# Optimization experiments

Hardware: AMD Instinct MI355X
Metric: run time of the kernel (lower is better)

The kernel has to match this reference:

```python
import jax, jax.numpy as jnp
import numpy as np

NUM_RING = 16
MAX_RING = 1520
EPS = 1e-5


def setup_inputs() -> dict:
    key = jax.random.key(0)
    B, C, N = 16, 64, 16384
    cnt = N // NUM_RING  # 1024 points per ring, sorted
    k1, k2, k3, k4, k5 = jax.random.split(key, 5)
    x = jax.random.normal(k1, (B, C, N), dtype=jnp.float32)
    # ring ids: sorted, exactly cnt points per ring (the module assumes sorted,
    # identical-count rings across batch)
    ring = jnp.broadcast_to(jnp.arange(N, dtype=jnp.int64) // cnt, (B, N))
    # random-upsample indices: concat(arange(cnt), randperm(cnt)[:MAX_RING-cnt])
    rng = np.random.default_rng(0)
    up = MAX_RING - cnt  # 496
    choice = np.empty((B, NUM_RING, MAX_RING), dtype=np.int64)
    for b in range(B):
        for r in range(NUM_RING):
            choice[b, r, :cnt] = np.arange(cnt)
            choice[b, r, cnt:] = rng.permutation(cnt)[:up]
    choice = jnp.asarray(choice)
    # grouped Conv1d(64 -> 128, kernel 1, groups=16): weight [128, 4, 1] -> [16, 8, 4]
    Wg = jax.random.normal(k2, (NUM_RING, 8, 4), dtype=jnp.float32) * 0.5
    bias = jax.random.normal(k3, (128,), dtype=jnp.float32) * 0.1
    gamma = jnp.ones((128,), dtype=jnp.float32)
    beta = jnp.zeros((128,), dtype=jnp.float32)
    return {"x": x, "Wg": Wg, "bias": bias, "gamma": gamma, "beta": beta,
            "ring": ring, "choice": choice}


def reference(x, Wg, bias, gamma, beta, ring, choice):
    B, C, N = x.shape  # C = 64
    R, MR = NUM_RING, MAX_RING
    cnt = N // R
    L = R * MR  # 24320

    xt = jnp.transpose(x, (0, 2, 1))  # [B, N, 64]
    # per-ring gather with random upsample to MAX_RING points
    idx = (jnp.arange(R, dtype=choice.dtype)[None, :, None] * cnt + choice)  # [B,R,MR]
    gathered = jnp.take_along_axis(xt, idx.reshape(B, L, 1), axis=1)  # [B, L, 64]

    # faithful to torch: cat(...).view(B, 64, -1) is a raw reshape (channel-scrambling)
    xc = gathered.reshape(B, C, L)  # [B, 64, L]

    # grouped 1x1 conv: 16 groups, 4 in / 8 out channels each
    xg = xc.reshape(B, R, 4, L)
    y = jnp.einsum('goc,bgcl->bgol', Wg, xg).reshape(B, 128, L)
    y = y + bias[None, :, None]

    # BatchNorm1d (training mode: batch statistics, biased variance)
    mean = jnp.mean(y, axis=(0, 2))
    var = jnp.var(y, axis=(0, 2))
    y = gamma[None, :, None] * (y - mean[None, :, None]) * jax.lax.rsqrt(var + EPS)[None, :, None] + beta[None, :, None]

    # per-ring max over MAX_RING slots, broadcast back to original ring sizes
    pooled = jnp.max(y.reshape(B, 128, R, MR), axis=-1)  # [B, 128, R]
    out = jnp.repeat(pooled, cnt, axis=2)  # [B, 128, N]
    return out
```

## Files before the change

kernel.cpp:

```cpp
#include <hip/hip_runtime.h>
#include <float.h>

#define NB    16
#define CIN   64
#define NPT   16384
#define NRING 16
#define MAXR  1520
#define LTOT  (NRING*MAXR)
#define MBLK  380
#define NCH   128
#define NBLK1 (NB*CIN*4)
#define MW    380

__device__ __forceinline__ float sload(float v) {
    return __int_as_float(__builtin_amdgcn_readfirstlane(__float_as_int(v)));
}

__global__ __launch_bounds__(256) void k1_gather_conv(
    const float* __restrict__ x, const float* __restrict__ Wg,
    const float* __restrict__ bias, const float* __restrict__ gamma,
    const int* __restrict__ choice,
    float* __restrict__ p_sum, float* __restrict__ p_sqs,
    float* __restrict__ p_max)
{
    __shared__ float xs[4096];
    __shared__ int   iw[4*MW];

    const int blk = blockIdx.x;
    const int b  = blk >> 8;
    const int cp = (blk >> 2) & 63;
    const int q  = blk & 3;
    const int t  = threadIdx.x;

    {
        const float4* src = (const float4*)(x + ((size_t)(b*CIN + cp)) * NPT + q*4096);
        float4* dst = (float4*)xs;
        #pragma unroll
        for (int i = 0; i < 4; ++i) dst[t + i*256] = src[t + i*256];
    }
    {
        const int g4 = t >> 6, lane = t & 63;
        const int* __restrict__ cg = choice + ((size_t)(b*NRING + q*4 + g4)) * MAXR;
        #pragma unroll
        for (int k = 0; k < 6; ++k) {
            const int m = lane + k*64;
            if (m < MW) {
                const int c2 = cg[760  + m];
                const int c3 = cg[1140 + m];
                iw[g4*MW + m] = c2 | (c3 << 16);
            }
        }
    }
    __syncthreads();

    const int g4   = t >> 6;
    const int lane = t & 63;
    const int r    = lane >> 2;
    const int s    = lane & 3;
    const int g    = q*4 + g4;

    float w[8][4], bs[8];
    #pragma unroll
    for (int o = 0; o < 8; ++o) {
        const int ch = g*8 + o;
        const float sg = (gamma[ch] < 0.0f) ? -1.0f : 1.0f;
        bs[o] = sload(sg * bias[ch]);
        #pragma unroll
        for (int c = 0; c < 4; ++c) w[o][c] = sload(sg * Wg[ch*4 + c]);
    }

    const int mlo = (r*MAXR - cp + 63) >> 6;
    int mhi = ((r+1)*MAXR - cp + 63) >> 6;
    if (mhi > MBLK) mhi = MBLK;

    const float* __restrict__ xg = xs + (g4 << 10);
    const int*   __restrict__ ig = iw + g4*MW;

    float smax[8], ssum[8], ssq[8];
    #pragma unroll
    for (int o = 0; o < 8; ++o) { smax[o] = -FLT_MAX; ssum[o] = 0.f; ssq[o] = 0.f; }

    const int m0 = mlo + s;

    int wv[5];
    #pragma unroll
    for (int k = 0; k < 5; ++k) wv[k] = ig[m0 + 4*k];

    #pragma unroll
    for (int k = 0; k < 5; ++k) {
        const int m = m0 + 4*k;
        const int i2 = wv[k] & 0xFFFF;
        const int i3 = ((unsigned)wv[k]) >> 16;
        const float v0 = xg[m];
        const float v1 = xg[380 + m];
        const float v2 = xg[i2];
        const float v3 = xg[i3];
        #pragma unroll
        for (int o = 0; o < 8; ++o) {
            float y = fmaf(w[o][0], v0, fmaf(w[o][1], v1,
                      fmaf(w[o][2], v2, fmaf(w[o][3], v3, bs[o]))));
            smax[o] = fmaxf(smax[o], y);
            ssum[o] += y;
            ssq[o]  = fmaf(y, y, ssq[o]);
        }
    }
    {
        const int m = m0 + 20;
        if (m < mhi) {
            const int wt = ig[m];
            const int i2 = wt & 0xFFFF;
            const int i3 = ((unsigned)wt) >> 16;
            const float v0 = xg[m];
            const float v1 = xg[380 + m];
            const float v2 = xg[i2];
            const float v3 = xg[i3];
            #pragma unroll
            for (int o = 0; o < 8; ++o) {
                float y = fmaf(w[o][0], v0, fmaf(w[o][1], v1,
                          fmaf(w[o][2], v2, fmaf(w[o][3], v3, bs[o]))));
                smax[o] = fmaxf(smax[o], y);
                ssum[o] += y;
                ssq[o]  = fmaf(y, y, ssq[o]);
            }
        }
    }

    #pragma unroll
    for (int o = 0; o < 8; ++o) {
        smax[o] = fmaxf(smax[o], __shfl_xor(smax[o], 1));
        ssum[o] += __shfl_xor(ssum[o], 1);
        ssq[o]  += __shfl_xor(ssq[o], 1);
        smax[o] = fmaxf(smax[o], __shfl_xor(smax[o], 2));
        ssum[o] += __shfl_xor(ssum[o], 2);
        ssq[o]  += __shfl_xor(ssq[o], 2);
    }

    if (s == 0) {
        float* base = p_max + (((size_t)(b*64 + cp))*NRING + r)*NCH + q*32 + g4*8;
        ((float4*)base)[0] = make_float4(smax[0], smax[1], smax[2], smax[3]);
        ((float4*)base)[1] = make_float4(smax[4], smax[5], smax[6], smax[7]);
    }

    __syncthreads();
    float* redS = xs;
    float* redQ = xs + 600;
    if (s == 0) {
        #pragma unroll
        for (int o = 0; o < 8; ++o) {
            redS[(g4*8+o)*17 + r] = ssum[o];
            redQ[(g4*8+o)*17 + r] = ssq[o];
        }
    }
    __syncthreads();
    if (t < 32) {
        float S = 0.f, Q = 0.f;
        #pragma unroll
        for (int rr = 0; rr < 16; ++rr) {
            S += redS[t*17 + rr];
            Q += redQ[t*17 + rr];
        }
        const float sg = (gamma[q*32 + t] < 0.0f) ? -1.0f : 1.0f;
        p_sum[(size_t)blk*32 + t] = sg * S;
        p_sqs[(size_t)blk*32 + t] = Q;
    }
}

__global__ __launch_bounds__(256) void k23_pool_bcast(
    const float* __restrict__ p_sum, const float* __restrict__ p_sqs,
    const float* __restrict__ p_max,
    const float* __restrict__ gamma, const float* __restrict__ beta,
    float4* __restrict__ out)
{
    __shared__ float part[16][17];
    __shared__ float wsum[4], wsq[4];
    __shared__ float pool[16];
    const int bc = blockIdx.x;
    const int b  = bc >> 7;
    const int ch = bc & 127;
    const int t  = threadIdx.x;
    const int q  = ch >> 5, c32 = ch & 31;

    const int r = t >> 4, ck = t & 15;
    float v = -FLT_MAX;
    #pragma unroll
    for (int k = 0; k < 4; ++k) {
        const int cpi = ck*4 + k;
        v = fmaxf(v, p_max[(((size_t)(b*64 + cpi))*NRING + r)*NCH + ch]);
    }

    float S = 0.f, Q = 0.f;
    #pragma unroll
    for (int i = 0; i < 4; ++i) {
        const int jj = t + i*256;
        const int b2 = jj >> 6, cp2 = jj & 63;
        const int kb = ((b2*64 + cp2) << 2) | q;
        S += p_sum[(size_t)kb*32 + c32];
        Q += p_sqs[(size_t)kb*32 + c32];
    }
    #pragma unroll
    for (int off = 1; off < 64; off <<= 1) {
        S += __shfl_xor(S, off);
        Q += __shfl_xor(Q, off);
    }
    part[r][ck] = v;
    if ((t & 63) == 0) { wsum[t >> 6] = S; wsq[t >> 6] = Q; }
    __syncthreads();

    if (t < 16) {
        const float inv = 1.0f / (float)((size_t)NB * LTOT);
        const float Sa = wsum[0] + wsum[1] + wsum[2] + wsum[3];
        const float Qa = wsq[0] + wsq[1] + wsq[2] + wsq[3];
        const float mean = Sa * inv;
        const float var  = Qa * inv - mean*mean;
        const float istd = rsqrtf(var + 1e-5f);
        float acc = part[t][0];
        #pragma unroll
        for (int k = 1; k < 16; ++k) acc = fmaxf(acc, part[t][k]);
        const float gm = gamma[ch];
        const float raw = (gm >= 0.0f) ? acc : -acc;
        pool[t] = gm * (raw - mean) * istd + beta[ch];
    }
    __syncthreads();

    float4* __restrict__ dst = out + (size_t)bc * (NPT/4);
    #pragma unroll
    for (int i = 0; i < 16; ++i) {
        const int idx = t + i*256;
        const float vv = pool[idx >> 8];
        dst[idx] = make_float4(vv, vv, vv, vv);
    }
}

extern "C" void kernel_launch(void* const* d_in, const int* in_sizes, int n_in,
                              void* d_out, int out_size, void* d_ws, size_t ws_size,
                              hipStream_t stream)
{
    const float* x     = (const float*)d_in[0];
    const float* Wg    = (const float*)d_in[1];
    const float* bias  = (const float*)d_in[2];
    const float* gamma = (const float*)d_in[3];
    const float* beta  = (const float*)d_in[4];
    const int* choice  = (const int*)d_in[6];

    float* p_sum = (float*)d_ws;
    float* p_sqs = p_sum + (size_t)NBLK1*32;
    float* p_max = p_sqs + (size_t)NBLK1*32;

    k1_gather_conv<<<NBLK1, 256, 0, stream>>>(x, Wg, bias, gamma, choice,
                                              p_sum, p_sqs, p_max);
    k23_pool_bcast<<<NB*NCH, 256, 0, stream>>>(p_sum, p_sqs, p_max,
                                               gamma, beta, (float4*)d_out);
}
```

Measured before the change: 66.39 us.

## Double-buffer x tiles via direct global-to-LDS loads and loop over channel slices

Restructures the gather-conv kernel from 4096 small 256-thread blocks into 512 blocks of 512 threads. Each block handles 8 ring groups and iterates over 4 input channel slices, reusing the loaded weights and choice indices across iterations. It double-buffers the x slices in LDS using the global_load_lds builtin, so the next slice loads while the current one is computed. Partial-sum reduction is moved to wave shuffles instead of a shared-memory pass, and the output broadcast uses nontemporal stores. The trade-offs are fewer blocks, which may leave CUs underfilled, and more LDS per block.

```diff
diff --git a/kernel.cpp b/kernel.cpp
--- a/kernel.cpp
+++ b/kernel.cpp
@@ -9,167 +9,192 @@
 #define LTOT  (NRING*MAXR)
 #define MBLK  380
 #define NCH   128
-#define NBLK1 (NB*CIN*4)
 #define MW    380
+
+typedef float fx4 __attribute__((ext_vector_type(4)));
 
 __device__ __forceinline__ float sload(float v) {
     return __int_as_float(__builtin_amdgcn_readfirstlane(__float_as_int(v)));
 }
 
-__global__ __launch_bounds__(256) void k1_gather_conv(
+#if __has_builtin(__builtin_amdgcn_global_load_lds)
+#define HAVE_GLDS 1
+__device__ __forceinline__ void gl_lds16(const float* g, float* l) {
+    __builtin_amdgcn_global_load_lds(
+        (const __attribute__((address_space(1))) void*)g,
+        (__attribute__((address_space(3))) void*)l, 16, 0, 0);
+}
+#else
+#define HAVE_GLDS 0
+#endif
+
+__global__ __launch_bounds__(512) void k1_gather_conv(
     const float* __restrict__ x, const float* __restrict__ Wg,
     const float* __restrict__ bias, const float* __restrict__ gamma,
     const int* __restrict__ choice,
     float* __restrict__ p_sum, float* __restrict__ p_sqs,
     float* __restrict__ p_max)
 {
-    __shared__ float xs[4096];
-    __shared__ int   iw[4*MW];
-
-    const int blk = blockIdx.x;
-    const int b  = blk >> 8;
-    const int cp = (blk >> 2) & 63;
-    const int q  = blk & 3;
-    const int t  = threadIdx.x;
+    __shared__ float xs[2][8192];
+    __shared__ int   iw[8*MW];
+
+    const int bid  = blockIdx.x;
+    const int bh    = bid >> 4;
+    const int slice = bid & 15;
+    const int b  = bh >> 1;
+    const int h  = bh & 1;
+    const int cp0 = slice << 2;
+    const int t    = threadIdx.x;
+    const int w    = t >> 6;
+    const int lane = t & 63;
+
+#if HAVE_GLDS
+    #define STAGE(bufi, cpv) do { \
+        const float* gb_ = x + ((size_t)(b*CIN + (cpv)))*NPT + h*8192 + w*1024 + lane*4; \
+        float* lb_ = &xs[bufi][w*1024]; \
+        gl_lds16(gb_,       lb_);       \
+        gl_lds16(gb_ + 256, lb_ + 256); \
+        gl_lds16(gb_ + 512, lb_ + 512); \
+        gl_lds16(gb_ + 768, lb_ + 768); \
+    } while (0)
+#else
+    #define STAGE(bufi, cpv) do { \
+        const fx4* src_ = (const fx4*)(x + ((size_t)(b*CIN + (cpv)))*NPT + h*8192); \
+        fx4* dst_ = (fx4*)xs[bufi]; \
+        _Pragma("unroll") \
+        for (int i_ = 0; i_ < 4; ++i_) dst_[t + i_*512] = src_[t + i_*512]; \
+    } while (0)
+#endif
+
+    STAGE(0, cp0);
 
     {
-        const float4* src = (const float4*)(x + ((size_t)(b*CIN + cp)) * NPT + q*4096);
-        float4* dst = (float4*)xs;
-        #pragma unroll
-        for (int i = 0; i < 4; ++i) dst[t + i*256] = src[t + i*256];
-    }
-    {
-        const int g4 = t >> 6, lane = t & 63;
-        const int* __restrict__ cg = choice + ((size_t)(b*NRING + q*4 + g4)) * MAXR;
+        const int* __restrict__ cg = choice + ((size_t)(b*NRING + h*8 + w))*MAXR;
         #pragma unroll
         for (int k = 0; k < 6; ++k) {
             const int m = lane + k*64;
-            if (m < MW) {
-                const int c2 = cg[760  + m];
-                const int c3 = cg[1140 + m];
-                iw[g4*MW + m] = c2 | (c3 << 16);
-            }
-        }
-    }
-    __syncthreads();
-
-    const int g4   = t >> 6;
-    const int lane = t & 63;
-    const int r    = lane >> 2;
-    const int s    = lane & 3;
-    const int g    = q*4 + g4;
-
-    float w[8][4], bs[8];
+            if (m < MW) iw[w*MW + m] = cg[760 + m] | (cg[1140 + m] << 16);
+        }
+    }
+
+    const int g = h*8 + w;
+    float wq[8][4], bq[8], sg8[8];
     #pragma unroll
     for (int o = 0; o < 8; ++o) {
         const int ch = g*8 + o;
-        const float sg = (gamma[ch] < 0.0f) ? -1.0f : 1.0f;
-        bs[o] = sload(sg * bias[ch]);
-        #pragma unroll
-        for (int c = 0; c < 4; ++c) w[o][c] = sload(sg * Wg[ch*4 + c]);
-    }
-
-    const int mlo = (r*MAXR - cp + 63) >> 6;
-    int mhi = ((r+1)*MAXR - cp + 63) >> 6;
-    if (mhi > MBLK) mhi = MBLK;
-
-    const float* __restrict__ xg = xs + (g4 << 10);
-    const int*   __restrict__ ig = iw + g4*MW;
-
-    float smax[8], ssum[8], ssq[8];
-    #pragma unroll
-    for (int o = 0; o < 8; ++o) { smax[o] = -FLT_MAX; ssum[o] = 0.f; ssq[o] = 0.f; }
-
-    const int m0 = mlo + s;
-
-    int wv[5];
-    #pragma unroll
-    for (int k = 0; k < 5; ++k) wv[k] = ig[m0 + 4*k];
-
-    #pragma unroll
-    for (int k = 0; k < 5; ++k) {
-        const int m = m0 + 4*k;
-        const int i2 = wv[k] & 0xFFFF;
-        const int i3 = ((unsigned)wv[k]) >> 16;
-        const float v0 = xg[m];
-        const float v1 = xg[380 + m];
-        const float v2 = xg[i2];
-        const float v3 = xg[i3];
-        #pragma unroll
-        for (int o = 0; o < 8; ++o) {
-            float y = fmaf(w[o][0], v0, fmaf(w[o][1], v1,
-                      fmaf(w[o][2], v2, fmaf(w[o][3], v3, bs[o]))));
-            smax[o] = fmaxf(smax[o], y);
-            ssum[o] += y;
-            ssq[o]  = fmaf(y, y, ssq[o]);
-        }
-    }
-    {
-        const int m = m0 + 20;
-        if (m < mhi) {
-            const int wt = ig[m];
-            const int i2 = wt & 0xFFFF;
-            const int i3 = ((unsigned)wt) >> 16;
+        const float sgn = (gamma[ch] < 0.0f) ? -1.0f : 1.0f;
+        sg8[o] = sload(sgn);
+        bq[o]  = sload(sgn * bias[ch]);
+        #pragma unroll
+        for (int c = 0; c < 4; ++c) wq[o][c] = sload(sgn * Wg[ch*4 + c]);
+    }
+
+    const int r = lane >> 2;
+    const int s = lane & 3;
+    const int* __restrict__ igw = iw + w*MW;
+
+    __syncthreads();
+
+    for (int tt = 0; tt < 4; ++tt) {
+        const int cp = cp0 + tt;
+        const float* __restrict__ xg = &xs[tt & 1][w << 10];
+        if (tt < 3) STAGE((tt + 1) & 1, cp + 1);
+
+        const int mlo = (r*MAXR - cp + 63) >> 6;
+        int mhi = ((r+1)*MAXR - cp + 63) >> 6;
+        if (mhi > MBLK) mhi = MBLK;
+        const int m0 = mlo + s;
+
+        int wv[5];
+        #pragma unroll
+        for (int k = 0; k < 5; ++k) wv[k] = igw[m0 + 4*k];
+
+        float smax[8], ssum[8], ssq[8];
+        #pragma unroll
+        for (int o = 0; o < 8; ++o) { smax[o] = -FLT_MAX; ssum[o] = 0.f; ssq[o] = 0.f; }
+
+        #pragma unroll
+        for (int k = 0; k < 5; ++k) {
+            const int m = m0 + 4*k;
+            const int i2 = wv[k] & 0xFFFF;
+            const int i3 = ((unsigned)wv[k]) >> 16;
             const float v0 = xg[m];
             const float v1 = xg[380 + m];
             const float v2 = xg[i2];
             const float v3 = xg[i3];
             #pragma unroll
             for (int o = 0; o < 8; ++o) {
-                float y = fmaf(w[o][0], v0, fmaf(w[o][1], v1,
-                          fmaf(w[o][2], v2, fmaf(w[o][3], v3, bs[o]))));
+                float y = fmaf(wq[o][0], v0, fmaf(wq[o][1], v1,
+                          fmaf(wq[o][2], v2, fmaf(wq[o][3], v3, bq[o]))));
                 smax[o] = fmaxf(smax[o], y);
                 ssum[o] += y;
                 ssq[o]  = fmaf(y, y, ssq[o]);
             }
         }
-    }
-
-    #pragma unroll
-    for (int o = 0; o < 8; ++o) {
-        smax[o] = fmaxf(smax[o], __shfl_xor(smax[o], 1));
-        ssum[o] += __shfl_xor(ssum[o], 1);
-        ssq[o]  += __shfl_xor(ssq[o], 1);
-        smax[o] = fmaxf(smax[o], __shfl_xor(smax[o], 2));
-        ssum[o] += __shfl_xor(ssum[o], 2);
-        ssq[o]  += __shfl_xor(ssq[o], 2);
-    }
-
-    if (s == 0) {
-        float* base = p_max + (((size_t)(b*64 + cp))*NRING + r)*NCH + q*32 + g4*8;
-        ((float4*)base)[0] = make_float4(smax[0], smax[1], smax[2], smax[3]);
-        ((float4*)base)[1] = make_float4(smax[4], smax[5], smax[6], smax[7]);
-    }
-
-    __syncthreads();
-    float* redS = xs;
-    float* redQ = xs + 600;
-    if (s == 0) {
+        {
+            const int m = m0 + 20;
+            if (m < mhi) {
+                const int wt = igw[m];
+                const int i2 = wt & 0xFFFF;
+                const int i3 = ((unsigned)wt) >> 16;
+                const float v0 = xg[m];
+                const float v1 = xg[380 + m];
+                const float v2 = xg[i2];
+                const float v3 = xg[i3];
+                #pragma unroll
+                for (int o = 0; o < 8; ++o) {
+                    float y = fmaf(wq[o][0], v0, fmaf(wq[o][1], v1,
+                              fmaf(wq[o][2], v2, fmaf(wq[o][3], v3, bq[o]))));
+                    smax[o] = fmaxf(smax[o], y);
+                    ssum[o] += y;
+                    ssq[o]  = fmaf(y, y, ssq[o]);
+                }
+            }
+        }
+
         #pragma unroll
         for (int o = 0; o < 8; ++o) {
-            redS[(g4*8+o)*17 + r] = ssum[o];
-            redQ[(g4*8+o)*17 + r] = ssq[o];
-        }
-    }
-    __syncthreads();
-    if (t < 32) {
-        float S = 0.f, Q = 0.f;
-        #pragma unroll
-        for (int rr = 0; rr < 16; ++rr) {
-            S += redS[t*17 + rr];
-            Q += redQ[t*17 + rr];
-        }
-        const float sg = (gamma[q*32 + t] < 0.0f) ? -1.0f : 1.0f;
-        p_sum[(size_t)blk*32 + t] = sg * S;
-        p_sqs[(size_t)blk*32 + t] = Q;
-    }
+            smax[o] = fmaxf(smax[o], __shfl_xor(smax[o], 1));
+            ssum[o] += __shfl_xor(ssum[o], 1);
+            ssq[o]  += __shfl_xor(ssq[o], 1);
+            smax[o] = fmaxf(smax[o], __shfl_xor(smax[o], 2));
+            ssum[o] += __shfl_xor(ssum[o], 2);
+            ssq[o]  += __shfl_xor(ssq[o], 2);
+        }
+
+        if (s == 0) {
+            float* base = p_max + (((size_t)(b*64 + cp))*NRING + r)*NCH + h*64 + w*8;
+            ((float4*)base)[0] = make_float4(smax[0], smax[1], smax[2], smax[3]);
+            ((float4*)base)[1] = make_float4(smax[4], smax[5], smax[6], smax[7]);
+        }
+
+        #pragma unroll
+        for (int o = 0; o < 8; ++o) {
+            #pragma unroll
+            for (int off = 4; off < 64; off <<= 1) {
+                ssum[o] += __shfl_xor(ssum[o], off);
+                ssq[o]  += __shfl_xor(ssq[o], off);
+            }
+        }
+        if (lane == 0) {
+            float* baseS = p_sum + ((size_t)((b*64 + cp)*2 + h))*64 + w*8;
+            float* baseQ = p_sqs + ((size_t)((b*64 + cp)*2 + h))*64 + w*8;
+            ((float4*)baseS)[0] = make_float4(sg8[0]*ssum[0], sg8[1]*ssum[1], sg8[2]*ssum[2], sg8[3]*ssum[3]);
+            ((float4*)baseS)[1] = make_float4(sg8[4]*ssum[4], sg8[5]*ssum[5], sg8[6]*ssum[6], sg8[7]*ssum[7]);
+            ((float4*)baseQ)[0] = make_float4(ssq[0], ssq[1], ssq[2], ssq[3]);
+            ((float4*)baseQ)[1] = make_float4(ssq[4], ssq[5], ssq[6], ssq[7]);
+        }
+
+        __syncthreads();
+    }
+    #undef STAGE
 }
 
 __global__ __launch_bounds__(256) void k23_pool_bcast(
     const float* __restrict__ p_sum, const float* __restrict__ p_sqs,
     const float* __restrict__ p_max,
     const float* __restrict__ gamma, const float* __restrict__ beta,
-    float4* __restrict__ out)
+    fx4* __restrict__ out)
 {
     __shared__ float part[16][17];
     __shared__ float wsum[4], wsq[4];
@@ -178,7 +203,7 @@
     const int b  = bc >> 7;
     const int ch = bc & 127;
     const int t  = threadIdx.x;
-    const int q  = ch >> 5, c32 = ch & 31;
+    const int hh = ch >> 6, c64 = ch & 63;
 
     const int r = t >> 4, ck = t & 15;
     float v = -FLT_MAX;
@@ -193,9 +218,9 @@
     for (int i = 0; i < 4; ++i) {
         const int jj = t + i*256;
         const int b2 = jj >> 6, cp2 = jj & 63;
-        const int kb = ((b2*64 + cp2) << 2) | q;
-        S += p_sum[(size_t)kb*32 + c32];
-        Q += p_sqs[(size_t)kb*32 + c32];
+        const int kb = b2*128 + cp2*2 + hh;
+        S += p_sum[(size_t)kb*64 + c64];
+        Q += p_sqs[(size_t)kb*64 + c64];
     }
     #pragma unroll
     for (int off = 1; off < 64; off <<= 1) {
@@ -222,12 +247,13 @@
     }
     __syncthreads();
 
-    float4* __restrict__ dst = out + (size_t)bc * (NPT/4);
+    fx4* __restrict__ dst = out + (size_t)bc * (NPT/4);
     #pragma unroll
     for (int i = 0; i < 16; ++i) {
         const int idx = t + i*256;
         const float vv = pool[idx >> 8];
-        dst[idx] = make_float4(vv, vv, vv, vv);
+        fx4 val; val.x = vv; val.y = vv; val.z = vv; val.w = vv;
+        __builtin_nontemporal_store(val, &dst[idx]);
     }
 }
 
@@ -243,11 +269,11 @@
     const int* choice  = (const int*)d_in[6];
 
     float* p_sum = (float*)d_ws;
-    float* p_sqs = p_sum + (size_t)NBLK1*32;
-    float* p_max = p_sqs + (size_t)NBLK1*32;
-
-    k1_gather_conv<<<NBLK1, 256, 0, stream>>>(x, Wg, bias, gamma, choice,
-                                              p_sum, p_sqs, p_max);
+    float* p_sqs = p_sum + (size_t)2048*64;
+    float* p_max = p_sqs + (size_t)2048*64;
+
+    k1_gather_conv<<<512, 512, 0, stream>>>(x, Wg, bias, gamma, choice,
+                                            p_sum, p_sqs, p_max);
     k23_pool_bcast<<<NB*NCH, 256, 0, stream>>>(p_sum, p_sqs, p_max,
-                                               gamma, beta, (float4*)d_out);
-}
+                                               gamma, beta, (fx4*)d_out);
+}
```

After: 71.72 us. 8.0% more time.
